# Performance work log

Hardware: AMD Instinct MI355X
Metric: run time of the kernel (lower is better)

## Reference

```python
import jax, jax.numpy as jnp
import numpy as np
from jax import lax


def _bilinear_sample(u, py, px):
    # u: [B,C,H,W]; py,px: [B,K,H,W] fractional coords; zero outside bounds
    H, W = u.shape[2], u.shape[3]
    y0 = jnp.floor(py)
    x0 = jnp.floor(px)
    y0i = y0.astype(jnp.int32)
    x0i = x0.astype(jnp.int32)
    wy1 = py - y0
    wy0 = 1.0 - wy1
    wx1 = px - x0
    wx0 = 1.0 - wx1

    def corner(yi, xi, w):
        valid = (yi >= 0) & (yi < H) & (xi >= 0) & (xi < W)
        yc = jnp.clip(yi, 0, H - 1)
        xc = jnp.clip(xi, 0, W - 1)
        # per-batch fancy gather: ub[:, y, x] -> [C,K,H,W]
        g = jax.vmap(lambda ub, y, x: ub[:, y, x])(u, yc, xc)  # [B,C,K,H,W]
        return g * (w * valid)[:, None]

    return (corner(y0i, x0i, wy0 * wx0)
            + corner(y0i, x0i + 1, wy0 * wx1)
            + corner(y0i + 1, x0i, wy1 * wx0)
            + corner(y0i + 1, x0i + 1, wy1 * wx1))


def _fam_forward(x, u, weight, bias, offset_w, offset_b):
    k = weight.shape[-1]
    pad = k // 2
    K = k * k
    B, C, H, W = u.shape
    # offset-predicting conv on concat(x, u), SAME padding
    concat = jnp.concatenate([x, u], axis=1)
    offset = lax.conv_general_dilated(concat, offset_w, (1, 1), [(pad, pad), (pad, pad)])
    offset = offset + offset_b[None, :, None, None]  # [B, 2K, H, W]
    off = offset.reshape(B, K, 2, H, W)
    dy = off[:, :, 0]
    dx = off[:, :, 1]
    ft = offset.dtype
    ki = jnp.arange(k, dtype=ft)
    ky = jnp.repeat(ki, k)  # [K] kernel row offsets
    kx = jnp.tile(ki, k)    # [K] kernel col offsets
    py = jnp.arange(H, dtype=ft)[None, None, :, None] - pad + ky[None, :, None, None] + dy
    px = jnp.arange(W, dtype=ft)[None, None, None, :] - pad + kx[None, :, None, None] + dx
    sampled = _bilinear_sample(u, py, px)  # [B,C,K,H,W]
    w = weight.reshape(weight.shape[0], weight.shape[1], K)  # [O,C,K]
    return jnp.einsum('bckhw,ock->bohw', sampled, w) + bias[None, :, None, None]


def setup_inputs() -> dict:
    key = jax.random.key(0)
    ks = jax.random.split(key, 4)
    B, Cx, Cu, H, W, k = 8, 128, 128, 64, 64, 3
    x = jax.random.normal(ks[0], (B, Cx, H, W), jnp.float32)
    u = jax.random.normal(ks[1], (B, Cu, H, W), jnp.float32)
    fan_in = Cu * k * k  # kaiming_uniform a=1 -> bound = sqrt(3/fan_in)
    bound = float(np.sqrt(3.0 / fan_in))
    weight = jax.random.uniform(ks[2], (Cu, Cu, k, k), jnp.float32, -bound, bound)
    bias = jnp.zeros((Cu,), jnp.float32)
    offset_w = jax.random.normal(ks[3], (2 * k * k, Cx + Cu, k, k), jnp.float32) * 0.01
    offset_b = jnp.zeros((2 * k * k,), jnp.float32)
    return {"x": x, "u": u, "weight": weight, "bias": bias,
            "offset_w": offset_w, "offset_b": offset_b}


def reference(x, u, weight, bias, offset_w, offset_b):
    return _fam_forward(x, u, weight, bias, offset_w, offset_b)
```

## Files before the change

### kernel.cpp

```cpp
#include <hip/hip_runtime.h>

#define BB 8
#define CC 128
#define HH 64
#define WW 64
#define NOFF 18

typedef __bf16 bf16x8 __attribute__((ext_vector_type(8)));
typedef float  f32x4  __attribute__((ext_vector_type(4)));
typedef float  f32x2u __attribute__((ext_vector_type(2), aligned(4)));

__global__ __launch_bounds__(256) void prep_transpose_kernel(
    const float* __restrict__ x, const float* __restrict__ u,
    const float* __restrict__ w, const float* __restrict__ ow,
    __bf16* __restrict__ ct, __bf16* __restrict__ af, __bf16* __restrict__ waf)
{
    const int tid = threadIdx.x;
    if (blockIdx.x < 512) {
        const int id   = blockIdx.x;
        const int b    = id & 7;
        const int y    = id >> 3;
        const int lane = tid & 63;
        const int wv   = tid >> 6;

        __shared__ __align__(16) __bf16 t[64][264];
#pragma unroll
        for (int g = 0; g < 8; ++g) {
            bf16x8 pk;
#pragma unroll
            for (int j = 0; j < 8; ++j) {
                int ic = wv * 64 + g * 8 + j;
                float v = (ic < CC)
                    ? x[((size_t)(b * CC + ic) * HH + y) * WW + lane]
                    : u[((size_t)(b * CC + (ic - CC)) * HH + y) * WW + lane];
                pk[j] = (__bf16)v;
            }
            *(bf16x8*)&t[lane][wv * 64 + g * 8] = pk;
        }
        __syncthreads();

        __bf16* dst = ct + (size_t)(b * HH + y) * WW * 256;
#pragma unroll
        for (int p = 0; p < 8; ++p) {
            int idx = p * 256 + tid;
            int px = idx >> 5, ch = idx & 31;
            *(bf16x8*)(dst + px * 256 + ch * 8) = *(const bf16x8*)&t[px][ch * 8];
        }
    } else {
        int idx = (blockIdx.x - 512) * 256 + tid;
        if (idx < 147456) {
            int j    = idx & 7;
            int lane = (idx >> 3) & 63;
            int ks   = (idx >> 9) & 3;
            int mt2  = (idx >> 11) & 7;
            int k    = idx >> 14;
            int o = mt2 * 16 + (lane & 15);
            int c = ks * 32 + (lane >> 4) * 8 + j;
            af[idx] = (__bf16)w[(o * CC + c) * 9 + k];
        } else if (idx < 147456 + 73728) {
            int t2   = idx - 147456;
            int j    = t2 & 7;
            int lane = (t2 >> 3) & 63;
            int ks   = (t2 >> 9) & 7;
            int mt   = (t2 >> 12) & 1;
            int kk   = t2 >> 13;
            int oc = mt * 16 + (lane & 15);
            int ic = ks * 32 + (lane >> 4) * 8 + j;
            float v = (oc < NOFF) ? ow[(oc * 256 + ic) * 9 + kk] : 0.f;
            waf[t2] = (__bf16)v;
        }
    }
}

__global__ __launch_bounds__(256, 2) void fam_fused_kernel(
    const __bf16* __restrict__ ct, const __bf16* __restrict__ waf,
    const __bf16* __restrict__ af, const float* __restrict__ ob,
    const float* __restrict__ bias, float* __restrict__ out)
{
    const int id   = blockIdx.x;
    const int b    = id & 7;
    const int h    = id >> 3;
    const int tid  = threadIdx.x;
    const int lane = tid & 63;
    const int wv   = tid >> 6;
    const int col  = lane & 15;
    const int quad = lane >> 4;

    __shared__ __align__(16) unsigned char smem[48640];
    __shared__ float off_lds[NOFF][64];

    __bf16 (*T)[264] = (__bf16(*)[264])smem;
    __bf16 (*sampT)[64][136] = (__bf16(*)[64][136])smem;
    float* s_ax = (float*)(smem + 34816);
    float* s_ay = s_ax + 576;
    float* s_bx = s_ay + 576;
    float* s_by = s_bx + 576;
    int*   s_i0 = (int*)(s_by + 576);
    int*   s_i1 = s_i0 + 576;

    {
        T[0][tid]  = (__bf16)0.f;
        T[65][tid] = (__bf16)0.f;

        f32x4 acc0 = {0.f, 0.f, 0.f, 0.f};
        f32x4 acc1 = {0.f, 0.f, 0.f, 0.f};
        const bf16x8* wafp = (const bf16x8*)waf;

        for (int kh = 0; kh < 3; ++kh) {
            int y = h - 1 + kh;
            if (y < 0 || y >= HH) continue;
            __syncthreads();
            const __bf16* row = ct + (size_t)(b * HH + y) * WW * 256;
#pragma unroll
            for (int p = 0; p < 8; ++p) {
                int idx = p * 256 + tid;
                int px = idx >> 5, ch = idx & 31;
                *(bf16x8*)&T[px + 1][ch * 8] =
                    *(const bf16x8*)(row + px * 256 + ch * 8);
            }
            __syncthreads();

#pragma unroll
            for (int kw = 0; kw < 3; ++kw) {
                int kk = kh * 3 + kw;
                const __bf16* brow = &T[wv * 16 + col + kw][quad * 8];
#pragma unroll
                for (int ks = 0; ks < 8; ++ks) {
                    bf16x8 bfrag = *(const bf16x8*)(brow + ks * 32);
                    bf16x8 a0 = wafp[((kk * 2 + 0) * 8 + ks) * 64 + lane];
                    bf16x8 a1 = wafp[((kk * 2 + 1) * 8 + ks) * 64 + lane];
                    acc0 = __builtin_amdgcn_mfma_f32_16x16x32_bf16(a0, bfrag, acc0, 0, 0, 0);
                    acc1 = __builtin_amdgcn_mfma_f32_16x16x32_bf16(a1, bfrag, acc1, 0, 0, 0);
                }
            }
        }

        int w2 = wv * 16 + col;
#pragma unroll
        for (int r = 0; r < 4; ++r)
            off_lds[quad * 4 + r][w2] = acc0[r] + ob[quad * 4 + r];
#pragma unroll
        for (int r = 0; r < 4; ++r) {
            int oc = 16 + quad * 4 + r;
            if (oc < NOFF) off_lds[oc][w2] = acc1[r] + ob[oc];
        }
    }
    __syncthreads();

    for (int t = tid; t < 9 * 64; t += 256) {
        int k  = t >> 6;
        int wq = t & 63;
        float dy = off_lds[2 * k][wq];
        float dx = off_lds[2 * k + 1][wq];
        float py = (float)(h - 1 + k / 3) + dy;
        float px = (float)(wq - 1 + k % 3) + dx;
        float y0f = floorf(py), x0f = floorf(px);
        int y0 = (int)y0f, x0 = (int)x0f;
        float fy = py - y0f, fx = px - x0f;
        bool vy0 = (y0 >= 0) && (y0 < HH);
        bool vy1 = (y0 + 1 >= 0) && (y0 + 1 < HH);
        bool vx0 = (x0 >= 0) && (x0 < WW);
        bool vx1 = (x0 + 1 >= 0) && (x0 + 1 < WW);
        float w00 = (1.f - fy) * (1.f - fx) * ((vy0 && vx0) ? 1.f : 0.f);
        float w01 = (1.f - fy) * fx         * ((vy0 && vx1) ? 1.f : 0.f);
        float w10 = fy * (1.f - fx)         * ((vy1 && vx0) ? 1.f : 0.f);
        float w11 = fy * fx                 * ((vy1 && vx1) ? 1.f : 0.f);
        int y0c = min(max(y0, 0), HH - 1);
        int y1c = min(max(y0 + 1, 0), HH - 1);
        int x0c = min(max(x0, 0), WW - 1);
        int x1c = min(max(x0 + 1, 0), WW - 1);
        int xl  = min(max(x0, 0), WW - 2);
        float ax = ((x0c == xl)     ? w00 : 0.f) + ((x1c == xl)     ? w01 : 0.f);
        float ay = ((x0c == xl + 1) ? w00 : 0.f) + ((x1c == xl + 1) ? w01 : 0.f);
        float bx = ((x0c == xl)     ? w10 : 0.f) + ((x1c == xl)     ? w11 : 0.f);
        float by = ((x0c == xl + 1) ? w10 : 0.f) + ((x1c == xl + 1) ? w11 : 0.f);
        s_ax[k * 64 + wq] = ax; s_ay[k * 64 + wq] = ay;
        s_bx[k * 64 + wq] = bx; s_by[k * 64 + wq] = by;
        s_i0[k * 64 + wq] = y0c * WW + xl;
        s_i1[k * 64 + wq] = y1c * WW + xl;
    }
    __syncthreads();

    f32x4 acc[2][4];
#pragma unroll
    for (int mt = 0; mt < 2; ++mt)
#pragma unroll
        for (int nt = 0; nt < 4; ++nt) acc[mt][nt] = (f32x4){0.f, 0.f, 0.f, 0.f};

    const __bf16* ctb = ct + (size_t)b * (HH * WW * 256);
    const bf16x8* afp = (const bf16x8*)af;

    bf16x8 rA[4], rB[4], rC[4], rD[4];

    auto preload = [&](int kk) {
#pragma unroll
        for (int p = 0; p < 4; ++p) {
            int idx = p * 256 + tid;
            int px = idx >> 4, ch = idx & 15;
            const __bf16* r0 = ctb + (size_t)s_i0[kk * 64 + px] * 256 + 128 + ch * 8;
            const __bf16* r1 = ctb + (size_t)s_i1[kk * 64 + px] * 256 + 128 + ch * 8;
            rA[p] = *(const bf16x8*)r0;
            rB[p] = *(const bf16x8*)(r0 + 256);
            rC[p] = *(const bf16x8*)r1;
            rD[p] = *(const bf16x8*)(r1 + 256);
        }
    };
    auto combine = [&](int kk, int buf) {
#pragma unroll
        for (int p = 0; p < 4; ++p) {
            int idx = p * 256 + tid;
            int px = idx >> 4, ch = idx & 15;
            float ax = s_ax[kk * 64 + px], ay = s_ay[kk * 64 + px];
            float bx = s_bx[kk * 64 + px], by = s_by[kk * 64 + px];
            bf16x8 res;
#pragma unroll
            for (int j = 0; j < 8; ++j)
                res[j] = (__bf16)(ax * (float)rA[p][j] + ay * (float)rB[p][j] +
                                  bx * (float)rC[p][j] + by * (float)rD[p][j]);
            *(bf16x8*)&sampT[buf][px][ch * 8] = res;
        }
    };
    auto domfma = [&](int kk, int buf) {
#pragma unroll
        for (int ks = 0; ks < 4; ++ks) {
            bf16x8 a0 = afp[((kk * 8 + wv * 2 + 0) * 4 + ks) * 64 + lane];
            bf16x8 a1 = afp[((kk * 8 + wv * 2 + 1) * 4 + ks) * 64 + lane];
            int crow = ks * 32 + quad * 8;
#pragma unroll
            for (int nt = 0; nt < 4; ++nt) {
                bf16x8 bfrag = *(const bf16x8*)&sampT[buf][nt * 16 + col][crow];
                acc[0][nt] = __builtin_amdgcn_mfma_f32_16x16x32_bf16(
                    a0, bfrag, acc[0][nt], 0, 0, 0);
                acc[1][nt] = __builtin_amdgcn_mfma_f32_16x16x32_bf16(
                    a1, bfrag, acc[1][nt], 0, 0, 0);
            }
        }
    };

    preload(0);
    combine(0, 0);
    preload(1);
    __syncthreads();
    for (int k = 0; k < 9; ++k) {
        domfma(k, k & 1);
        if (k < 8) {
            combine(k + 1, (k + 1) & 1);
            if (k + 2 <= 8) preload(k + 2);
            __syncthreads();
        }
    }

#pragma unroll
    for (int mt = 0; mt < 2; ++mt) {
#pragma unroll
        for (int r = 0; r < 4; ++r) {
            int o = wv * 32 + mt * 16 + quad * 4 + r;
            float bv = bias[o];
#pragma unroll
            for (int nt = 0; nt < 4; ++nt)
                out[((size_t)(b * CC + o) * HH + h) * WW + nt * 16 + col] =
                    acc[mt][nt][r] + bv;
        }
    }
}

__global__ __launch_bounds__(256) void prep_kernel(
    const float* __restrict__ w, const float* __restrict__ ow,
    __bf16* __restrict__ af, __bf16* __restrict__ waf)
{
    int idx = blockIdx.x * 256 + threadIdx.x;
    if (idx < 147456) {
        int j    = idx & 7;
        int lane = (idx >> 3) & 63;
        int ks   = (idx >> 9) & 3;
        int mt2  = (idx >> 11) & 7;
        int k    = idx >> 14;
        int o = mt2 * 16 + (lane & 15);
        int c = ks * 32 + (lane >> 4) * 8 + j;
        af[idx] = (__bf16)w[(o * CC + c) * 9 + k];
    } else if (idx < 147456 + 73728) {
        int t    = idx - 147456;
        int j    = t & 7;
        int lane = (t >> 3) & 63;
        int ks   = (t >> 9) & 7;
        int mt   = (t >> 12) & 1;
        int kk   = t >> 13;
        int oc = mt * 16 + (lane & 15);
        int ic = ks * 32 + (lane >> 4) * 8 + j;
        float v = (oc < NOFF) ? ow[(oc * 256 + ic) * 9 + kk] : 0.f;
        waf[t] = (__bf16)v;
    }
}

#define TS 264
__global__ __launch_bounds__(256) void offset_conv_mfma_kernel(
    const float* __restrict__ x, const float* __restrict__ u,
    const __bf16* __restrict__ waf, const float* __restrict__ ob,
    float* __restrict__ off)
{
    const int id   = blockIdx.x;
    const int b    = id & 7;
    const int h    = id >> 3;
    const int tid  = threadIdx.x;
    const int lane = tid & 63;
    const int wv   = tid >> 6;
    const int col  = lane & 15;
    const int quad = lane >> 4;

    __shared__ __align__(16) __bf16 T[66][TS];
    {
        T[0][tid]  = (__bf16)0.f;
        T[65][tid] = (__bf16)0.f;
    }

    f32x4 acc0 = {0.f, 0.f, 0.f, 0.f};
    f32x4 acc1 = {0.f, 0.f, 0.f, 0.f};
    const bf16x8* wafp = (const bf16x8*)waf;

    for (int kh = 0; kh < 3; ++kh) {
        int y = h - 1 + kh;
        if (y < 0 || y >= HH) continue;
        __syncthreads();
        {
            int w2 = lane;
#pragma unroll
            for (int g = 0; g < 8; ++g) {
                bf16x8 pk;
#pragma unroll
                for (int j = 0; j < 8; ++j) {
                    int ic = wv * 64 + g * 8 + j;
                    float v = (ic < CC)
                        ? x[((size_t)(b * CC + ic) * HH + y) * WW + w2]
                        : u[((size_t)(b * CC + (ic - CC)) * HH + y) * WW + w2];
                    pk[j] = (__bf16)v;
                }
                *(bf16x8*)&T[w2 + 1][wv * 64 + g * 8] = pk;
            }
        }
        __syncthreads();

#pragma unroll
        for (int kw = 0; kw < 3; ++kw) {
            int kk = kh * 3 + kw;
            const __bf16* brow = &T[wv * 16 + col + kw][quad * 8];
#pragma unroll
            for (int ks = 0; ks < 8; ++ks) {
                bf16x8 bfrag = *(const bf16x8*)(brow + ks * 32);
                bf16x8 a0 = wafp[((kk * 2 + 0) * 8 + ks) * 64 + lane];
                bf16x8 a1 = wafp[((kk * 2 + 1) * 8 + ks) * 64 + lane];
                acc0 = __builtin_amdgcn_mfma_f32_16x16x32_bf16(a0, bfrag, acc0, 0, 0, 0);
                acc1 = __builtin_amdgcn_mfma_f32_16x16x32_bf16(a1, bfrag, acc1, 0, 0, 0);
            }
        }
    }

    int w2 = wv * 16 + col;
#pragma unroll
    for (int r = 0; r < 4; ++r) {
        int oc = quad * 4 + r;
        off[((size_t)(b * NOFF + oc) * HH + h) * WW + w2] = acc0[r] + ob[oc];
    }
#pragma unroll
    for (int r = 0; r < 4; ++r) {
        int oc = 16 + quad * 4 + r;
        if (oc < NOFF)
            off[((size_t)(b * NOFF + oc) * HH + h) * WW + w2] = acc1[r] + ob[oc];
    }
}

__global__ __launch_bounds__(256) void fam_main_kernel(
    const float* __restrict__ u, const __bf16* __restrict__ af,
    const float* __restrict__ bias, const float* __restrict__ off,
    float* __restrict__ out)
{
    const int id   = blockIdx.x;
    const int b    = id & 7;
    const int h    = id >> 3;
    const int tid  = threadIdx.x;
    const int lane = tid & 63;
    const int wv   = tid >> 6;
    const int col  = lane & 15;
    const int quad = lane >> 4;

    __shared__ __align__(16) __bf16 sampT[64][136];
    __shared__ float s_ax[9][64], s_ay[9][64], s_bx[9][64], s_by[9][64];
    __shared__ int   s_i0[9][64], s_i1[9][64];

    for (int t = tid; t < 9 * 64; t += 256) {
        int k  = t >> 6;
        int wq = t & 63;
        float dy = off[((size_t)(b * NOFF + 2 * k)     * HH + h) * WW + wq];
        float dx = off[((size_t)(b * NOFF + 2 * k + 1) * HH + h) * WW + wq];
        float py = (float)(h - 1 + k / 3) + dy;
        float px = (float)(wq - 1 + k % 3) + dx;
        float y0f = floorf(py), x0f = floorf(px);
        int y0 = (int)y0f, x0 = (int)x0f;
        float fy = py - y0f, fx = px - x0f;
        bool vy0 = (y0 >= 0) && (y0 < HH);
        bool vy1 = (y0 + 1 >= 0) && (y0 + 1 < HH);
        bool vx0 = (x0 >= 0) && (x0 < WW);
        bool vx1 = (x0 + 1 >= 0) && (x0 + 1 < WW);
        float w00 = (1.f - fy) * (1.f - fx) * ((vy0 && vx0) ? 1.f : 0.f);
        float w01 = (1.f - fy) * fx         * ((vy0 && vx1) ? 1.f : 0.f);
        float w10 = fy * (1.f - fx)         * ((vy1 && vx0) ? 1.f : 0.f);
        float w11 = fy * fx                 * ((vy1 && vx1) ? 1.f : 0.f);
        int y0c = min(max(y0, 0), HH - 1);
        int y1c = min(max(y0 + 1, 0), HH - 1);
        int x0c = min(max(x0, 0), WW - 1);
        int x1c = min(max(x0 + 1, 0), WW - 1);
        int xl  = min(max(x0, 0), WW - 2);
        float ax = ((x0c == xl)     ? w00 : 0.f) + ((x1c == xl)     ? w01 : 0.f);
        float ay = ((x0c == xl + 1) ? w00 : 0.f) + ((x1c == xl + 1) ? w01 : 0.f);
        float bx = ((x0c == xl)     ? w10 : 0.f) + ((x1c == xl)     ? w11 : 0.f);
        float by = ((x0c == xl + 1) ? w10 : 0.f) + ((x1c == xl + 1) ? w11 : 0.f);
        s_ax[k][wq] = ax; s_ay[k][wq] = ay;
        s_bx[k][wq] = bx; s_by[k][wq] = by;
        s_i0[k][wq] = y0c * WW + xl;
        s_i1[k][wq] = y1c * WW + xl;
    }
    __syncthreads();

    f32x4 acc[2][4];
#pragma unroll
    for (int mt = 0; mt < 2; ++mt)
#pragma unroll
        for (int nt = 0; nt < 4; ++nt) acc[mt][nt] = (f32x4){0.f, 0.f, 0.f, 0.f};

    const float* ub = u + (size_t)b * (CC * HH * WW);
    const bf16x8* afp = (const bf16x8*)af;

    for (int k = 0; k < 9; ++k) {
        {
            float ax = s_ax[k][lane], ay = s_ay[k][lane];
            float bx = s_bx[k][lane], by = s_by[k][lane];
            int   i0 = s_i0[k][lane], i1 = s_i1[k][lane];
#pragma unroll 4
            for (int g = 0; g < 4; ++g) {
                bf16x8 pk;
#pragma unroll
                for (int j = 0; j < 8; ++j) {
                    const float* up = ub + (size_t)(wv * 32 + g * 8 + j) * (HH * WW);
                    f32x2u r0 = *(const f32x2u*)(up + i0);
                    f32x2u r1 = *(const f32x2u*)(up + i1);
                    float v = ax * r0.x + ay * r0.y + bx * r1.x + by * r1.y;
                    pk[j] = (__bf16)v;
                }
                *(bf16x8*)&sampT[lane][wv * 32 + g * 8] = pk;
            }
        }
        __syncthreads();

#pragma unroll
        for (int ks = 0; ks < 4; ++ks) {
            bf16x8 a0 = afp[((k * 8 + wv * 2 + 0) * 4 + ks) * 64 + lane];
            bf16x8 a1 = afp[((k * 8 + wv * 2 + 1) * 4 + ks) * 64 + lane];
            int crow = ks * 32 + quad * 8;
#pragma unroll
            for (int nt = 0; nt < 4; ++nt) {
                bf16x8 bfrag = *(const bf16x8*)&sampT[nt * 16 + col][crow];
                acc[0][nt] = __builtin_amdgcn_mfma_f32_16x16x32_bf16(
                    a0, bfrag, acc[0][nt], 0, 0, 0);
                acc[1][nt] = __builtin_amdgcn_mfma_f32_16x16x32_bf16(
                    a1, bfrag, acc[1][nt], 0, 0, 0);
            }
        }
        __syncthreads();
    }

#pragma unroll
    for (int mt = 0; mt < 2; ++mt) {
#pragma unroll
        for (int r = 0; r < 4; ++r) {
            int o = wv * 32 + mt * 16 + quad * 4 + r;
            float bv = bias[o];
#pragma unroll
            for (int nt = 0; nt < 4; ++nt)
                out[((size_t)(b * CC + o) * HH + h) * WW + nt * 16 + col] =
                    acc[mt][nt][r] + bv;
        }
    }
}

extern "C" void kernel_launch(void* const* d_in, const int* in_sizes, int n_in,
                              void* d_out, int out_size, void* d_ws, size_t ws_size,
                              hipStream_t stream) {
    const float* x    = (const float*)d_in[0];
    const float* u    = (const float*)d_in[1];
    const float* wgt  = (const float*)d_in[2];
    const float* bias = (const float*)d_in[3];
    const float* ow   = (const float*)d_in[4];
    const float* ob   = (const float*)d_in[5];
    float* out = (float*)d_out;

    float*  off = (float*)d_ws;
    __bf16* af  = (__bf16*)(off + (size_t)BB * NOFF * HH * WW);
    __bf16* waf = af + 147456;
    __bf16* ct  = waf + 73728;
    const size_t need_fast = 2359296 + 294912 + 147456 + (size_t)BB * HH * WW * 256 * 2;

    if (ws_size >= need_fast) {
        hipLaunchKernelGGL(prep_transpose_kernel, dim3(1376), dim3(256), 0, stream,
                           x, u, wgt, ow, ct, af, waf);
        hipLaunchKernelGGL(fam_fused_kernel, dim3(512), dim3(256), 0, stream,
                           ct, waf, af, ob, bias, out);
    } else {
        hipLaunchKernelGGL(prep_kernel, dim3(864), dim3(256), 0, stream,
                           wgt, ow, af, waf);
        hipLaunchKernelGGL(offset_conv_mfma_kernel, dim3(512), dim3(256), 0, stream,
                           x, u, waf, ob, off);
        hipLaunchKernelGGL(fam_main_kernel, dim3(512), dim3(256), 0, stream,
                           u, af, bias, off, out);
    }
}
```

Measured before the change: 129.8 us.

## Split each output row across two blocks to double grid and occupancy

Result: slower. 134.5 us (+3.6%).

```diff
diff --git a/kernel.cpp b/kernel.cpp
--- a/kernel.cpp
+++ b/kernel.cpp
@@ -72,38 +72,38 @@
     }
 }
 
-__global__ __launch_bounds__(256, 2) void fam_fused_kernel(
+__global__ __launch_bounds__(256, 4) void fam_fused_kernel(
     const __bf16* __restrict__ ct, const __bf16* __restrict__ waf,
     const __bf16* __restrict__ af, const float* __restrict__ ob,
     const float* __restrict__ bias, float* __restrict__ out)
 {
     const int id   = blockIdx.x;
     const int b    = id & 7;
-    const int h    = id >> 3;
+    const int half = (id >> 3) & 1;
+    const int h    = id >> 4;
+    const int p0   = half * 32;
     const int tid  = threadIdx.x;
     const int lane = tid & 63;
     const int wv   = tid >> 6;
     const int col  = lane & 15;
     const int quad = lane >> 4;
 
-    __shared__ __align__(16) unsigned char smem[48640];
-    __shared__ float off_lds[NOFF][64];
+    __shared__ __align__(16) unsigned char smem[24320];
+    __shared__ float off_lds[NOFF][32];
 
     __bf16 (*T)[264] = (__bf16(*)[264])smem;
-    __bf16 (*sampT)[64][136] = (__bf16(*)[64][136])smem;
-    float* s_ax = (float*)(smem + 34816);
-    float* s_ay = s_ax + 576;
-    float* s_bx = s_ay + 576;
-    float* s_by = s_bx + 576;
-    int*   s_i0 = (int*)(s_by + 576);
-    int*   s_i1 = s_i0 + 576;
+    __bf16 (*sampT)[32][136] = (__bf16(*)[32][136])smem;
+    float* s_ax = (float*)(smem + 17408);
+    float* s_ay = s_ax + 288;
+    float* s_bx = s_ay + 288;
+    float* s_by = s_bx + 288;
+    int*   s_i0 = (int*)(s_by + 288);
+    int*   s_i1 = s_i0 + 288;
 
     {
-        T[0][tid]  = (__bf16)0.f;
-        T[65][tid] = (__bf16)0.f;
-
-        f32x4 acc0 = {0.f, 0.f, 0.f, 0.f};
-        f32x4 acc1 = {0.f, 0.f, 0.f, 0.f};
+        const int mt  = wv >> 1;
+        const int ntw = wv & 1;
+        f32x4 acc = {0.f, 0.f, 0.f, 0.f};
         const bf16x8* wafp = (const bf16x8*)waf;
 
         for (int kh = 0; kh < 3; ++kh) {
@@ -112,48 +112,53 @@
             __syncthreads();
             const __bf16* row = ct + (size_t)(b * HH + y) * WW * 256;
 #pragma unroll
-            for (int p = 0; p < 8; ++p) {
-                int idx = p * 256 + tid;
-                int px = idx >> 5, ch = idx & 31;
-                *(bf16x8*)&T[px + 1][ch * 8] =
-                    *(const bf16x8*)(row + px * 256 + ch * 8);
+            for (int it = 0; it < 5; ++it) {
+                int idx = it * 256 + tid;
+                if (idx < 34 * 32) {
+                    int cl = idx >> 5, ch = idx & 31;
+                    int gpx = p0 - 1 + cl;
+                    bf16x8 v;
+                    if (gpx >= 0 && gpx < WW)
+                        v = *(const bf16x8*)(row + gpx * 256 + ch * 8);
+                    else {
+#pragma unroll
+                        for (int j = 0; j < 8; ++j) v[j] = (__bf16)0.f;
+                    }
+                    *(bf16x8*)&T[cl][ch * 8] = v;
+                }
             }
             __syncthreads();
 
 #pragma unroll
             for (int kw = 0; kw < 3; ++kw) {
                 int kk = kh * 3 + kw;
-                const __bf16* brow = &T[wv * 16 + col + kw][quad * 8];
+                const __bf16* brow = &T[ntw * 16 + col + kw][quad * 8];
 #pragma unroll
                 for (int ks = 0; ks < 8; ++ks) {
                     bf16x8 bfrag = *(const bf16x8*)(brow + ks * 32);
-                    bf16x8 a0 = wafp[((kk * 2 + 0) * 8 + ks) * 64 + lane];
-                    bf16x8 a1 = wafp[((kk * 2 + 1) * 8 + ks) * 64 + lane];
-                    acc0 = __builtin_amdgcn_mfma_f32_16x16x32_bf16(a0, bfrag, acc0, 0, 0, 0);
-                    acc1 = __builtin_amdgcn_mfma_f32_16x16x32_bf16(a1, bfrag, acc1, 0, 0, 0);
+                    bf16x8 a = wafp[((kk * 2 + mt) * 8 + ks) * 64 + lane];
+                    acc = __builtin_amdgcn_mfma_f32_16x16x32_bf16(a, bfrag, acc, 0, 0, 0);
                 }
             }
         }
 
-        int w2 = wv * 16 + col;
-#pragma unroll
-        for (int r = 0; r < 4; ++r)
-            off_lds[quad * 4 + r][w2] = acc0[r] + ob[quad * 4 + r];
+        int pxl = ntw * 16 + col;
 #pragma unroll
         for (int r = 0; r < 4; ++r) {
-            int oc = 16 + quad * 4 + r;
-            if (oc < NOFF) off_lds[oc][w2] = acc1[r] + ob[oc];
+            int oc = mt * 16 + quad * 4 + r;
+            if (oc < NOFF) off_lds[oc][pxl] = acc[r] + ob[oc];
         }
     }
     __syncthreads();
 
-    for (int t = tid; t < 9 * 64; t += 256) {
-        int k  = t >> 6;
-        int wq = t & 63;
+    for (int t = tid; t < 9 * 32; t += 256) {
+        int k  = t >> 5;
+        int wq = t & 31;
+        int wqg = p0 + wq;
         float dy = off_lds[2 * k][wq];
         float dx = off_lds[2 * k + 1][wq];
         float py = (float)(h - 1 + k / 3) + dy;
-        float px = (float)(wq - 1 + k % 3) + dx;
+        float px = (float)(wqg - 1 + k % 3) + dx;
         float y0f = floorf(py), x0f = floorf(px);
         int y0 = (int)y0f, x0 = (int)x0f;
         float fy = py - y0f, fx = px - x0f;
@@ -174,31 +179,31 @@
         float ay = ((x0c == xl + 1) ? w00 : 0.f) + ((x1c == xl + 1) ? w01 : 0.f);
         float bx = ((x0c == xl)     ? w10 : 0.f) + ((x1c == xl)     ? w11 : 0.f);
         float by = ((x0c == xl + 1) ? w10 : 0.f) + ((x1c == xl + 1) ? w11 : 0.f);
-        s_ax[k * 64 + wq] = ax; s_ay[k * 64 + wq] = ay;
-        s_bx[k * 64 + wq] = bx; s_by[k * 64 + wq] = by;
-        s_i0[k * 64 + wq] = y0c * WW + xl;
-        s_i1[k * 64 + wq] = y1c * WW + xl;
+        s_ax[k * 32 + wq] = ax; s_ay[k * 32 + wq] = ay;
+        s_bx[k * 32 + wq] = bx; s_by[k * 32 + wq] = by;
+        s_i0[k * 32 + wq] = y0c * WW + xl;
+        s_i1[k * 32 + wq] = y1c * WW + xl;
     }
     __syncthreads();
 
-    f32x4 acc[2][4];
+    f32x4 acc[2][2];
 #pragma unroll
     for (int mt = 0; mt < 2; ++mt)
 #pragma unroll
-        for (int nt = 0; nt < 4; ++nt) acc[mt][nt] = (f32x4){0.f, 0.f, 0.f, 0.f};
+        for (int nt = 0; nt < 2; ++nt) acc[mt][nt] = (f32x4){0.f, 0.f, 0.f, 0.f};
 
     const __bf16* ctb = ct + (size_t)b * (HH * WW * 256);
     const bf16x8* afp = (const bf16x8*)af;
 
-    bf16x8 rA[4], rB[4], rC[4], rD[4];
+    bf16x8 rA[2], rB[2], rC[2], rD[2];
 
     auto preload = [&](int kk) {
 #pragma unroll
-        for (int p = 0; p < 4; ++p) {
+        for (int p = 0; p < 2; ++p) {
             int idx = p * 256 + tid;
             int px = idx >> 4, ch = idx & 15;
-            const __bf16* r0 = ctb + (size_t)s_i0[kk * 64 + px] * 256 + 128 + ch * 8;
-            const __bf16* r1 = ctb + (size_t)s_i1[kk * 64 + px] * 256 + 128 + ch * 8;
+            const __bf16* r0 = ctb + (size_t)s_i0[kk * 32 + px] * 256 + 128 + ch * 8;
+            const __bf16* r1 = ctb + (size_t)s_i1[kk * 32 + px] * 256 + 128 + ch * 8;
             rA[p] = *(const bf16x8*)r0;
             rB[p] = *(const bf16x8*)(r0 + 256);
             rC[p] = *(const bf16x8*)r1;
@@ -207,11 +212,11 @@
     };
     auto combine = [&](int kk, int buf) {
 #pragma unroll
-        for (int p = 0; p < 4; ++p) {
+        for (int p = 0; p < 2; ++p) {
             int idx = p * 256 + tid;
             int px = idx >> 4, ch = idx & 15;
-            float ax = s_ax[kk * 64 + px], ay = s_ay[kk * 64 + px];
-            float bx = s_bx[kk * 64 + px], by = s_by[kk * 64 + px];
+            float ax = s_ax[kk * 32 + px], ay = s_ay[kk * 32 + px];
+            float bx = s_bx[kk * 32 + px], by = s_by[kk * 32 + px];
             bf16x8 res;
 #pragma unroll
             for (int j = 0; j < 8; ++j)
@@ -227,7 +232,7 @@
             bf16x8 a1 = afp[((kk * 8 + wv * 2 + 1) * 4 + ks) * 64 + lane];
             int crow = ks * 32 + quad * 8;
 #pragma unroll
-            for (int nt = 0; nt < 4; ++nt) {
+            for (int nt = 0; nt < 2; ++nt) {
                 bf16x8 bfrag = *(const bf16x8*)&sampT[buf][nt * 16 + col][crow];
                 acc[0][nt] = __builtin_amdgcn_mfma_f32_16x16x32_bf16(
                     a0, bfrag, acc[0][nt], 0, 0, 0);
@@ -257,8 +262,8 @@
             int o = wv * 32 + mt * 16 + quad * 4 + r;
             float bv = bias[o];
 #pragma unroll
-            for (int nt = 0; nt < 4; ++nt)
-                out[((size_t)(b * CC + o) * HH + h) * WW + nt * 16 + col] =
+            for (int nt = 0; nt < 2; ++nt)
+                out[((size_t)(b * CC + o) * HH + h) * WW + p0 + nt * 16 + col] =
                     acc[mt][nt][r] + bv;
         }
     }
@@ -501,7 +506,7 @@
     if (ws_size >= need_fast) {
         hipLaunchKernelGGL(prep_transpose_kernel, dim3(1376), dim3(256), 0, stream,
                            x, u, wgt, ow, ct, af, waf);
-        hipLaunchKernelGGL(fam_fused_kernel, dim3(512), dim3(256), 0, stream,
+        hipLaunchKernelGGL(fam_fused_kernel, dim3(1024), dim3(256), 0, stream,
                            ct, waf, af, ob, bias, out);
     } else {
         hipLaunchKernelGGL(prep_kernel, dim3(864), dim3(256), 0, stream,
```
